# Performance work log

Hardware: AMD Instinct MI355X
Metric: run time of the kernel (lower is better)

Reference implementation:

```python
import jax, jax.numpy as jnp
import numpy as np

B = 64          # number of trees (batch)
N = 131072      # total nodes in batch
H_ENC = 512
H_DEC = 512


def setup_inputs() -> dict:
    key = jax.random.key(0)
    k1, k2, k3, k4, k5 = jax.random.split(key, 5)
    hidden_states = jax.random.normal(k1, (B, H_DEC), dtype=jnp.float32)
    encoder_output = jax.random.normal(k2, (N, H_ENC), dtype=jnp.float32)
    # sorted segment ids encode ragged tree membership (same info as tree_sizes)
    segment_ids = jnp.sort(jax.random.randint(k3, (N,), 0, B)).astype(jnp.int32)
    # linear: nn.Linear(h_dec + h_enc, h_enc, bias=False) -> weight [h_enc, h_dec+h_enc]
    W = jax.random.normal(k4, (H_ENC, H_DEC + H_ENC), dtype=jnp.float32) / np.float32(np.sqrt(H_DEC + H_ENC))
    # v: torch.rand(h_enc, 1)
    v = jax.random.uniform(k5, (H_ENC, 1), dtype=jnp.float32)
    return {"hidden_states": hidden_states, "encoder_output": encoder_output,
            "segment_ids": segment_ids, "W": W, "v": v}


def reference(hidden_states, encoder_output, segment_ids, W, v):
    # repeat each tree's decoder state over its nodes: [N, h_dec]
    repeated = hidden_states[segment_ids]
    # concat score: tanh(Linear([h_dec ; h_enc])) @ v
    cat = jnp.concatenate([repeated, encoder_output], axis=1)      # [N, h_dec+h_enc]
    energy = jnp.tanh(cat @ W.T)                                   # [N, h_enc]
    scores = energy @ v                                            # [N, 1]
    s = scores[:, 0]
    # segment-wise (per-tree) softmax over ragged node groups
    seg_max = jax.ops.segment_max(s, segment_ids, num_segments=B)
    e = jnp.exp(s - seg_max[segment_ids])
    denom = jax.ops.segment_sum(e, segment_ids, num_segments=B)
    att = e / denom[segment_ids]
    return att[:, None]                                            # [N, 1]
```

## Files before the change

### kernel.cpp

```cpp
#include <hip/hip_runtime.h>
#include <math.h>

#define NROWS 131072
#define NSEG  64
#define HH    512

typedef unsigned short u16;
typedef unsigned int   u32;
typedef __attribute__((ext_vector_type(8))) short short8;
typedef __attribute__((ext_vector_type(8))) u16   us8;
typedef __attribute__((ext_vector_type(4))) float f32x4;
typedef __attribute__((ext_vector_type(4))) u32   u32x4;

__device__ __forceinline__ u32 f2u(float f){ union {float f; u32 u;} c; c.f=f; return c.u; }
__device__ __forceinline__ float u2f(u32 u){ union {u32 u; float f;} c; c.u=u; return c.f; }
__device__ __forceinline__ u16 bf16_rne(float f){
  u32 u = f2u(f);
  u32 r = u + 0x7FFFu + ((u >> 16) & 1u);
  return (u16)(r >> 16);
}
__device__ __forceinline__ float fast_tanh(float x){
  float e = __expf(2.0f * x);
  return 1.0f - __fdividef(2.0f, e + 1.0f);
}
__device__ __forceinline__ void gload_lds16(const void* g, void* l) {
  __builtin_amdgcn_global_load_lds((const __attribute__((address_space(1))) void*)g,
                                   (__attribute__((address_space(3))) void*)l, 16, 0, 0);
}

__global__ __launch_bounds__(256)
void hproj_kernel(const float* __restrict__ hidden, const float* __restrict__ W,
                  float* __restrict__ hproj)
{
  const int b    = blockIdx.x >> 2;
  const int q    = blockIdx.x & 3;
  const int tid  = threadIdx.x;
  const int wave = tid >> 6;
  const int lane = tid & 63;
  const float* hrow = hidden + (size_t)b * HH + lane * 8;
  const float4 h0 = *(const float4*)(hrow);
  const float4 h1 = *(const float4*)(hrow + 4);
  for (int j = q * 128 + wave; j < q * 128 + 128; j += 4) {
    const float* wrow = W + (size_t)j * 1024 + lane * 8;
    const float4 w0 = *(const float4*)(wrow);
    const float4 w1 = *(const float4*)(wrow + 4);
    float acc = h0.x*w0.x + h0.y*w0.y + h0.z*w0.z + h0.w*w0.w
              + h1.x*w1.x + h1.y*w1.y + h1.z*w1.z + h1.w*w1.w;
    #pragma unroll
    for (int o = 32; o; o >>= 1) acc += __shfl_xor(acc, o);
    if (lane == 0) hproj[(size_t)b * HH + j] = acc;
  }
}

__global__ __launch_bounds__(256)
void w2split_kernel(const float* __restrict__ W, u16* __restrict__ hi, u16* __restrict__ lo)
{
  const int idx = blockIdx.x * 256 + threadIdx.x;
  const int j = idx >> 9, k = idx & 511;
  const float x = W[(size_t)j * 1024 + 512 + k];
  const u32 u = f2u(x);
  hi[idx] = (u16)(u >> 16);
  lo[idx] = bf16_rne(x - u2f(u & 0xFFFF0000u));
}

__global__ __launch_bounds__(256, 2)
void gemm_fused_kernel(const float* __restrict__ enc,
                       const u16* __restrict__ w2hi, const u16* __restrict__ w2lo,
                       const float* __restrict__ hproj, const float* __restrict__ vvec,
                       const int* __restrict__ seg, float* __restrict__ scores)
{
  __shared__ float sAf[128 * 32];
  __shared__ u16   sBh[256 * 32];
  __shared__ u16   sBl[256 * 32];

  const int tid  = threadIdx.x;
  const int bx   = blockIdx.x;
  const int row0 = (bx >> 1) * 128;
  const int col0 = (bx & 1) * 256;

  const int wave = tid >> 6;
  const int lane = tid & 63;
  const int wrow = (wave >> 1) * 64;
  const int wcol = (wave & 1) * 128;
  const int l15  = lane & 15;
  const int quad = lane >> 4;

  const int arow = tid >> 3;
  const int acol = ((tid & 7) ^ (arow & 6)) * 4;
  const float* gA = enc + (size_t)(row0 + arow) * HH + acol;
  const int awb = (tid >> 6) * 256;

  const int brow = tid >> 2;
  const int bcol = ((tid & 3) ^ ((brow >> 1) & 3)) * 8;
  const u16* gBh = w2hi + (size_t)(col0 + brow) * HH + bcol;
  const u16* gBl = w2lo + (size_t)(col0 + brow) * HH + bcol;
  const int bwb = (tid >> 6) * 512;

  f32x4 acc[4][8];
  #pragma unroll
  for (int i = 0; i < 4; i++)
    #pragma unroll
    for (int j = 0; j < 8; j++)
      acc[i][j] = (f32x4){0.f, 0.f, 0.f, 0.f};

  for (int ks = 0; ks < HH; ks += 32) {
    #pragma unroll
    for (int i = 0; i < 4; i++)
      gload_lds16(gA + (size_t)i * 32 * HH + ks, &sAf[i * 1024 + awb]);
    #pragma unroll
    for (int i = 0; i < 4; i++)
      gload_lds16(gBh + (size_t)i * 64 * HH + ks, &sBh[i * 2048 + bwb]);
    #pragma unroll
    for (int i = 0; i < 4; i++)
      gload_lds16(gBl + (size_t)i * 64 * HH + ks, &sBl[i * 2048 + bwb]);
    __syncthreads();

    short8 ah[4], al[4];
    #pragma unroll
    for (int i = 0; i < 4; i++) {
      const int r  = wrow + i * 16 + l15;
      const int ab = r * 32 + (((2 * quad) ^ (r & 6))) * 4;
      const f32x4 x0 = *(const f32x4*)&sAf[ab];
      const f32x4 x1 = *(const f32x4*)&sAf[ab + 4];
      union { u32x4 w; short8 s; } H, L;
      #pragma unroll
      for (int p = 0; p < 4; p++) {
        const float xa = (p < 2) ? x0[2 * p] : x1[2 * p - 4];
        const float xb = (p < 2) ? x0[2 * p + 1] : x1[2 * p - 3];
        const u32 ua = f2u(xa), ub = f2u(xb);
        H.w[p] = __builtin_amdgcn_perm(ub, ua, 0x07060302u);
        const float ra = xa - u2f(ua & 0xFFFF0000u);
        const float rb = xb - u2f(ub & 0xFFFF0000u);
        L.w[p] = __builtin_amdgcn_perm(f2u(rb), f2u(ra), 0x07060302u);
      }
      ah[i] = H.s;
      al[i] = L.s;
    }

    #pragma unroll
    for (int j = 0; j < 8; j++) {
      const int rr  = wcol + j * 16 + l15;
      const int off = rr * 32 + (quad ^ ((rr >> 1) & 3)) * 8;
      const short8 bh = *(const short8*)&sBh[off];
      const short8 bl = *(const short8*)&sBl[off];
      #pragma unroll
      for (int i = 0; i < 4; i++) {
        acc[i][j] = __builtin_amdgcn_mfma_f32_16x16x32_bf16(ah[i], bh, acc[i][j], 0, 0, 0);
        acc[i][j] = __builtin_amdgcn_mfma_f32_16x16x32_bf16(al[i], bh, acc[i][j], 0, 0, 0);
        acc[i][j] = __builtin_amdgcn_mfma_f32_16x16x32_bf16(ah[i], bl, acc[i][j], 0, 0, 0);
      }
    }
    __syncthreads();
  }

  int   jn[8];
  float vv[8];
  #pragma unroll
  for (int j = 0; j < 8; j++) { jn[j] = col0 + wcol + j * 16 + l15; vv[j] = vvec[jn[j]]; }

  #pragma unroll
  for (int i = 0; i < 4; i++) {
    #pragma unroll
    for (int r = 0; r < 4; r++) {
      const int gn = row0 + wrow + i * 16 + quad * 4 + r;
      const float* hp = hproj + (size_t)seg[gn] * HH;
      float p = 0.f;
      #pragma unroll
      for (int j = 0; j < 8; j++) {
        const float c = acc[i][j][r] + hp[jn[j]];
        p += fast_tanh(c) * vv[j];
      }
      p += __shfl_xor(p, 1);
      p += __shfl_xor(p, 2);
      p += __shfl_xor(p, 4);
      p += __shfl_xor(p, 8);
      if (l15 == 0) atomicAdd(&scores[gn], p);
    }
  }
}

__global__ __launch_bounds__(256)
void seg_softmax_kernel(const float* __restrict__ scores, const int* __restrict__ seg,
                        float* __restrict__ out)
{
  const int b    = blockIdx.x;
  const int tid  = threadIdx.x;
  const int wv   = tid >> 6;
  const int lane = tid & 63;
  __shared__ float red[4];

  int lo = 0, hi = NROWS;
  while (lo < hi) { int mid = (lo + hi) >> 1; if (seg[mid] < b) lo = mid + 1; else hi = mid; }
  const int start = lo;
  lo = 0; hi = NROWS;
  while (lo < hi) { int mid = (lo + hi) >> 1; if (seg[mid] < b + 1) lo = mid + 1; else hi = mid; }
  const int end = lo;

  float lm = -3.4e38f;
  for (int i = start + tid; i < end; i += 256) lm = fmaxf(lm, scores[i]);
  #pragma unroll
  for (int o = 32; o; o >>= 1) lm = fmaxf(lm, __shfl_xor(lm, o));
  if (lane == 0) red[wv] = lm;
  __syncthreads();
  const float gm = fmaxf(fmaxf(red[0], red[1]), fmaxf(red[2], red[3]));
  __syncthreads();

  float ls = 0.f;
  for (int i = start + tid; i < end; i += 256) ls += expf(scores[i] - gm);
  #pragma unroll
  for (int o = 32; o; o >>= 1) ls += __shfl_xor(ls, o);
  if (lane == 0) red[wv] = ls;
  __syncthreads();
  const float denom = red[0] + red[1] + red[2] + red[3];
  const float inv = 1.0f / denom;

  for (int i = start + tid; i < end; i += 256) out[i] = expf(scores[i] - gm) * inv;
}

extern "C" void kernel_launch(void* const* d_in, const int* in_sizes, int n_in,
                              void* d_out, int out_size, void* d_ws, size_t ws_size,
                              hipStream_t stream)
{
  const float* hidden = (const float*)d_in[0];
  const float* enc    = (const float*)d_in[1];
  const int*   seg    = (const int*)d_in[2];
  const float* W      = (const float*)d_in[3];
  const float* vvec   = (const float*)d_in[4];
  float* out = (float*)d_out;

  float* scores = (float*)d_ws;
  float* hproj  = scores + NROWS;
  u16*   w2hi   = (u16*)(hproj + NSEG * HH);
  u16*   w2lo   = w2hi + (size_t)HH * HH;

  hipMemsetAsync(scores, 0, NROWS * sizeof(float), stream);
  hproj_kernel<<<NSEG * 4, 256, 0, stream>>>(hidden, W, hproj);
  w2split_kernel<<<(HH * HH) / 256, 256, 0, stream>>>(W, w2hi, w2lo);
  gemm_fused_kernel<<<(NROWS / 128) * 2, 256, 0, stream>>>(enc, w2hi, w2lo,
                                                           hproj, vvec, seg, scores);
  seg_softmax_kernel<<<NSEG, 256, 0, stream>>>(scores, seg, out);
}
```

Before: 543.1 us.

## Double-buffer pre-converted bf16 A tiles in LDS and load B directly from global

Replaces the global_load_lds staging of fp32 A and the bf16 hi/lo B tiles. A is now prefetched into registers, split once into bf16 hi/lo and written to a double-buffered, padded LDS tile (LDA=40), so one sync per k-step overlaps the next tile's global load with the current MFMAs. Each wave reads its B fragments straight from global memory, which the small, cache-resident W2 allows. The aim is to stop every wave from redoing the A split and to overlap loads with compute, at the cost of more registers for prefetch and B fragments and more global/L2 traffic for B.

Result: slower. 674.1 us (+24.1%).

```diff
diff --git a/kernel.cpp b/kernel.cpp
--- a/kernel.cpp
+++ b/kernel.cpp
@@ -4,6 +4,7 @@
 #define NROWS 131072
 #define NSEG  64
 #define HH    512
+#define LDA   40
 
 typedef unsigned short u16;
 typedef unsigned int   u32;
@@ -22,10 +23,6 @@
 __device__ __forceinline__ float fast_tanh(float x){
   float e = __expf(2.0f * x);
   return 1.0f - __fdividef(2.0f, e + 1.0f);
-}
-__device__ __forceinline__ void gload_lds16(const void* g, void* l) {
-  __builtin_amdgcn_global_load_lds((const __attribute__((address_space(1))) void*)g,
-                                   (__attribute__((address_space(3))) void*)l, 16, 0, 0);
 }
 
 __global__ __launch_bounds__(256)
@@ -63,15 +60,31 @@
   lo[idx] = bf16_rne(x - u2f(u & 0xFFFF0000u));
 }
 
+__device__ __forceinline__ void convert_write(const float* pf, u16* dh, u16* dl)
+{
+  union { u32x4 w; us8 s; } H0, H1, L0, L1;
+  #pragma unroll
+  for (int p = 0; p < 8; p++) {
+    const float xa = pf[2 * p], xb = pf[2 * p + 1];
+    const u32 ua = f2u(xa), ub = f2u(xb);
+    const u32 h = __builtin_amdgcn_perm(ub, ua, 0x07060302u);
+    const float ra = xa - u2f(ua & 0xFFFF0000u);
+    const float rb = xb - u2f(ub & 0xFFFF0000u);
+    const u32 l = __builtin_amdgcn_perm(f2u(rb), f2u(ra), 0x07060302u);
+    if (p < 4) { H0.w[p] = h; L0.w[p] = l; } else { H1.w[p - 4] = h; L1.w[p - 4] = l; }
+  }
+  *(us8*)(dh)     = H0.s;  *(us8*)(dh + 8) = H1.s;
+  *(us8*)(dl)     = L0.s;  *(us8*)(dl + 8) = L1.s;
+}
+
 __global__ __launch_bounds__(256, 2)
 void gemm_fused_kernel(const float* __restrict__ enc,
                        const u16* __restrict__ w2hi, const u16* __restrict__ w2lo,
                        const float* __restrict__ hproj, const float* __restrict__ vvec,
                        const int* __restrict__ seg, float* __restrict__ scores)
 {
-  __shared__ float sAf[128 * 32];
-  __shared__ u16   sBh[256 * 32];
-  __shared__ u16   sBl[256 * 32];
+  __shared__ u16 sAh[2][128 * LDA];
+  __shared__ u16 sAl[2][128 * LDA];
 
   const int tid  = threadIdx.x;
   const int bx   = blockIdx.x;
@@ -85,16 +98,16 @@
   const int l15  = lane & 15;
   const int quad = lane >> 4;
 
-  const int arow = tid >> 3;
-  const int acol = ((tid & 7) ^ (arow & 6)) * 4;
-  const float* gA = enc + (size_t)(row0 + arow) * HH + acol;
-  const int awb = (tid >> 6) * 256;
-
-  const int brow = tid >> 2;
-  const int bcol = ((tid & 3) ^ ((brow >> 1) & 3)) * 8;
-  const u16* gBh = w2hi + (size_t)(col0 + brow) * HH + bcol;
-  const u16* gBl = w2lo + (size_t)(col0 + brow) * HH + bcol;
-  const int bwb = (tid >> 6) * 512;
+  const int sr = tid >> 1;
+  const int sh = (tid & 1) * 16;
+  const float* gA = enc + (size_t)(row0 + sr) * HH + sh;
+  u16* const dh0 = &sAh[0][sr * LDA + sh];
+  u16* const dl0 = &sAl[0][sr * LDA + sh];
+  u16* const dh1 = &sAh[1][sr * LDA + sh];
+  u16* const dl1 = &sAl[1][sr * LDA + sh];
+
+  const u16* gBh = w2hi + (size_t)(col0 + wcol + l15) * HH + quad * 8;
+  const u16* gBl = w2lo + (size_t)(col0 + wcol + l15) * HH + quad * 8;
 
   f32x4 acc[4][8];
   #pragma unroll
@@ -103,51 +116,48 @@
     for (int j = 0; j < 8; j++)
       acc[i][j] = (f32x4){0.f, 0.f, 0.f, 0.f};
 
+  float pf[16];
+  #pragma unroll
+  for (int q = 0; q < 4; q++) *(float4*)&pf[4 * q] = *(const float4*)(gA + 4 * q);
+  convert_write(pf, dh0, dl0);
+  #pragma unroll
+  for (int q = 0; q < 4; q++) *(float4*)&pf[4 * q] = *(const float4*)(gA + 32 + 4 * q);
+  __syncthreads();
+
   for (int ks = 0; ks < HH; ks += 32) {
-    #pragma unroll
-    for (int i = 0; i < 4; i++)
-      gload_lds16(gA + (size_t)i * 32 * HH + ks, &sAf[i * 1024 + awb]);
-    #pragma unroll
-    for (int i = 0; i < 4; i++)
-      gload_lds16(gBh + (size_t)i * 64 * HH + ks, &sBh[i * 2048 + bwb]);
-    #pragma unroll
-    for (int i = 0; i < 4; i++)
-      gload_lds16(gBl + (size_t)i * 64 * HH + ks, &sBl[i * 2048 + bwb]);
-    __syncthreads();
-
-    short8 ah[4], al[4];
-    #pragma unroll
-    for (int i = 0; i < 4; i++) {
-      const int r  = wrow + i * 16 + l15;
-      const int ab = r * 32 + (((2 * quad) ^ (r & 6))) * 4;
-      const f32x4 x0 = *(const f32x4*)&sAf[ab];
-      const f32x4 x1 = *(const f32x4*)&sAf[ab + 4];
-      union { u32x4 w; short8 s; } H, L;
+    const int cur = (ks >> 5) & 1;
+    const u16* cAh = sAh[cur];
+    const u16* cAl = sAl[cur];
+
+    if (ks + 32 < HH) {
+      convert_write(pf, cur ? dh0 : dh1, cur ? dl0 : dl1);
+      if (ks + 64 < HH) {
+        #pragma unroll
+        for (int q = 0; q < 4; q++)
+          *(float4*)&pf[4 * q] = *(const float4*)(gA + ks + 64 + 4 * q);
+      }
+    }
+
+    #pragma unroll
+    for (int jb = 0; jb < 2; jb++) {
+      short8 bh4[4], bl4[4];
       #pragma unroll
-      for (int p = 0; p < 4; p++) {
-        const float xa = (p < 2) ? x0[2 * p] : x1[2 * p - 4];
-        const float xb = (p < 2) ? x0[2 * p + 1] : x1[2 * p - 3];
-        const u32 ua = f2u(xa), ub = f2u(xb);
-        H.w[p] = __builtin_amdgcn_perm(ub, ua, 0x07060302u);
-        const float ra = xa - u2f(ua & 0xFFFF0000u);
-        const float rb = xb - u2f(ub & 0xFFFF0000u);
-        L.w[p] = __builtin_amdgcn_perm(f2u(rb), f2u(ra), 0x07060302u);
-      }
-      ah[i] = H.s;
-      al[i] = L.s;
-    }
-
-    #pragma unroll
-    for (int j = 0; j < 8; j++) {
-      const int rr  = wcol + j * 16 + l15;
-      const int off = rr * 32 + (quad ^ ((rr >> 1) & 3)) * 8;
-      const short8 bh = *(const short8*)&sBh[off];
-      const short8 bl = *(const short8*)&sBl[off];
+      for (int j = 0; j < 4; j++) {
+        const size_t off = (size_t)(jb * 4 + j) * 16 * HH + ks;
+        bh4[j] = *(const short8*)(gBh + off);
+        bl4[j] = *(const short8*)(gBl + off);
+      }
       #pragma unroll
       for (int i = 0; i < 4; i++) {
-        acc[i][j] = __builtin_amdgcn_mfma_f32_16x16x32_bf16(ah[i], bh, acc[i][j], 0, 0, 0);
-        acc[i][j] = __builtin_amdgcn_mfma_f32_16x16x32_bf16(al[i], bh, acc[i][j], 0, 0, 0);
-        acc[i][j] = __builtin_amdgcn_mfma_f32_16x16x32_bf16(ah[i], bl, acc[i][j], 0, 0, 0);
+        const int ar = (wrow + i * 16 + l15) * LDA + quad * 8;
+        const short8 ah = *(const short8*)&cAh[ar];
+        const short8 al = *(const short8*)&cAl[ar];
+        #pragma unroll
+        for (int j = 0; j < 4; j++) {
+          acc[i][jb * 4 + j] = __builtin_amdgcn_mfma_f32_16x16x32_bf16(ah, bh4[j], acc[i][jb * 4 + j], 0, 0, 0);
+          acc[i][jb * 4 + j] = __builtin_amdgcn_mfma_f32_16x16x32_bf16(al, bh4[j], acc[i][jb * 4 + j], 0, 0, 0);
+          acc[i][jb * 4 + j] = __builtin_amdgcn_mfma_f32_16x16x32_bf16(ah, bl4[j], acc[i][jb * 4 + j], 0, 0, 0);
+        }
       }
     }
     __syncthreads();
```

## Double-buffer GEMM LDS tiles, load low-weight bf16 to registers, drop atomics

Applied to the files above, without the earlier changes.

The GEMM main loop now double-buffers the encoder and high-part weight tiles in LDS, issuing the next K-slice's async loads before computing the current one. The low-part weight fragments are read straight from global memory into registers, also prefetched one step ahead, so LDS use drops. Per-wave partial scores go to four separate buffers summed in the softmax kernel, replacing atomics and the memset. The two prep kernels are merged into one launch. In exchange the kernel uses more registers and the softmax reads four times as much score data.

New measurement: 588.5 us. +8.4%, slower.

```diff
diff --git a/kernel.cpp b/kernel.cpp
--- a/kernel.cpp
+++ b/kernel.cpp
@@ -29,12 +29,22 @@
 }
 
 __global__ __launch_bounds__(256)
-void hproj_kernel(const float* __restrict__ hidden, const float* __restrict__ W,
-                  float* __restrict__ hproj)
-{
-  const int b    = blockIdx.x >> 2;
-  const int q    = blockIdx.x & 3;
-  const int tid  = threadIdx.x;
+void prep_kernel(const float* __restrict__ hidden, const float* __restrict__ W,
+                 float* __restrict__ hproj, u16* __restrict__ w2hi, u16* __restrict__ w2lo)
+{
+  const int tid = threadIdx.x;
+  if (blockIdx.x < 1024) {
+    const int idx = blockIdx.x * 256 + tid;
+    const int j = idx >> 9, k = idx & 511;
+    const float x = W[(size_t)j * 1024 + 512 + k];
+    const u32 u = f2u(x);
+    w2hi[idx] = (u16)(u >> 16);
+    w2lo[idx] = bf16_rne(x - u2f(u & 0xFFFF0000u));
+    return;
+  }
+  const int bq   = blockIdx.x - 1024;
+  const int b    = bq >> 2;
+  const int q    = bq & 3;
   const int wave = tid >> 6;
   const int lane = tid & 63;
   const float* hrow = hidden + (size_t)b * HH + lane * 8;
@@ -52,26 +62,14 @@
   }
 }
 
-__global__ __launch_bounds__(256)
-void w2split_kernel(const float* __restrict__ W, u16* __restrict__ hi, u16* __restrict__ lo)
-{
-  const int idx = blockIdx.x * 256 + threadIdx.x;
-  const int j = idx >> 9, k = idx & 511;
-  const float x = W[(size_t)j * 1024 + 512 + k];
-  const u32 u = f2u(x);
-  hi[idx] = (u16)(u >> 16);
-  lo[idx] = bf16_rne(x - u2f(u & 0xFFFF0000u));
-}
-
 __global__ __launch_bounds__(256, 2)
 void gemm_fused_kernel(const float* __restrict__ enc,
                        const u16* __restrict__ w2hi, const u16* __restrict__ w2lo,
                        const float* __restrict__ hproj, const float* __restrict__ vvec,
-                       const int* __restrict__ seg, float* __restrict__ scores)
-{
-  __shared__ float sAf[128 * 32];
-  __shared__ u16   sBh[256 * 32];
-  __shared__ u16   sBl[256 * 32];
+                       const int* __restrict__ seg, float* __restrict__ part)
+{
+  __shared__ float sAf[2][128 * 32];
+  __shared__ u16   sBh[2][256 * 32];
 
   const int tid  = threadIdx.x;
   const int bx   = blockIdx.x;
@@ -93,8 +91,9 @@
   const int brow = tid >> 2;
   const int bcol = ((tid & 3) ^ ((brow >> 1) & 3)) * 8;
   const u16* gBh = w2hi + (size_t)(col0 + brow) * HH + bcol;
-  const u16* gBl = w2lo + (size_t)(col0 + brow) * HH + bcol;
   const int bwb = (tid >> 6) * 512;
+
+  const u16* gBl = w2lo + (size_t)(col0 + wcol + l15) * HH + quad * 8;
 
   f32x4 acc[4][8];
   #pragma unroll
@@ -103,25 +102,41 @@
     for (int j = 0; j < 8; j++)
       acc[i][j] = (f32x4){0.f, 0.f, 0.f, 0.f};
 
+  #pragma unroll
+  for (int i = 0; i < 4; i++)
+    gload_lds16(gA + (size_t)i * 32 * HH, &sAf[0][i * 1024 + awb]);
+  #pragma unroll
+  for (int i = 0; i < 4; i++)
+    gload_lds16(gBh + (size_t)i * 64 * HH, &sBh[0][i * 2048 + bwb]);
+  short8 blC[8], blN[8];
+  #pragma unroll
+  for (int j = 0; j < 8; j++)
+    blC[j] = *(const short8*)(gBl + (size_t)j * 16 * HH);
+  __syncthreads();
+
   for (int ks = 0; ks < HH; ks += 32) {
-    #pragma unroll
-    for (int i = 0; i < 4; i++)
-      gload_lds16(gA + (size_t)i * 32 * HH + ks, &sAf[i * 1024 + awb]);
-    #pragma unroll
-    for (int i = 0; i < 4; i++)
-      gload_lds16(gBh + (size_t)i * 64 * HH + ks, &sBh[i * 2048 + bwb]);
-    #pragma unroll
-    for (int i = 0; i < 4; i++)
-      gload_lds16(gBl + (size_t)i * 64 * HH + ks, &sBl[i * 2048 + bwb]);
-    __syncthreads();
+    const int cur = (ks >> 5) & 1;
+    const int nxt = cur ^ 1;
+
+    if (ks + 32 < HH) {
+      #pragma unroll
+      for (int i = 0; i < 4; i++)
+        gload_lds16(gA + (size_t)i * 32 * HH + ks + 32, &sAf[nxt][i * 1024 + awb]);
+      #pragma unroll
+      for (int i = 0; i < 4; i++)
+        gload_lds16(gBh + (size_t)i * 64 * HH + ks + 32, &sBh[nxt][i * 2048 + bwb]);
+      #pragma unroll
+      for (int j = 0; j < 8; j++)
+        blN[j] = *(const short8*)(gBl + (size_t)j * 16 * HH + ks + 32);
+    }
 
     short8 ah[4], al[4];
     #pragma unroll
     for (int i = 0; i < 4; i++) {
       const int r  = wrow + i * 16 + l15;
       const int ab = r * 32 + (((2 * quad) ^ (r & 6))) * 4;
-      const f32x4 x0 = *(const f32x4*)&sAf[ab];
-      const f32x4 x1 = *(const f32x4*)&sAf[ab + 4];
+      const f32x4 x0 = *(const f32x4*)&sAf[cur][ab];
+      const f32x4 x1 = *(const f32x4*)&sAf[cur][ab + 4];
       union { u32x4 w; short8 s; } H, L;
       #pragma unroll
       for (int p = 0; p < 4; p++) {
@@ -141,8 +156,8 @@
     for (int j = 0; j < 8; j++) {
       const int rr  = wcol + j * 16 + l15;
       const int off = rr * 32 + (quad ^ ((rr >> 1) & 3)) * 8;
-      const short8 bh = *(const short8*)&sBh[off];
-      const short8 bl = *(const short8*)&sBl[off];
+      const short8 bh = *(const short8*)&sBh[cur][off];
+      const short8 bl = blC[j];
       #pragma unroll
       for (int i = 0; i < 4; i++) {
         acc[i][j] = __builtin_amdgcn_mfma_f32_16x16x32_bf16(ah[i], bh, acc[i][j], 0, 0, 0);
@@ -151,6 +166,8 @@
       }
     }
     __syncthreads();
+    #pragma unroll
+    for (int j = 0; j < 8; j++) blC[j] = blN[j];
   }
 
   int   jn[8];
@@ -158,6 +175,7 @@
   #pragma unroll
   for (int j = 0; j < 8; j++) { jn[j] = col0 + wcol + j * 16 + l15; vv[j] = vvec[jn[j]]; }
 
+  float* pout = part + (size_t)((bx & 1) * 2 + (wave & 1)) * NROWS;
   #pragma unroll
   for (int i = 0; i < 4; i++) {
     #pragma unroll
@@ -174,13 +192,13 @@
       p += __shfl_xor(p, 2);
       p += __shfl_xor(p, 4);
       p += __shfl_xor(p, 8);
-      if (l15 == 0) atomicAdd(&scores[gn], p);
+      if (l15 == 0) pout[gn] = p;
     }
   }
 }
 
 __global__ __launch_bounds__(256)
-void seg_softmax_kernel(const float* __restrict__ scores, const int* __restrict__ seg,
+void seg_softmax_kernel(const float* __restrict__ part, const int* __restrict__ seg,
                         float* __restrict__ out)
 {
   const int b    = blockIdx.x;
@@ -197,7 +215,10 @@
   const int end = lo;
 
   float lm = -3.4e38f;
-  for (int i = start + tid; i < end; i += 256) lm = fmaxf(lm, scores[i]);
+  for (int i = start + tid; i < end; i += 256) {
+    const float s = part[i] + part[NROWS + i] + part[2 * NROWS + i] + part[3 * NROWS + i];
+    lm = fmaxf(lm, s);
+  }
   #pragma unroll
   for (int o = 32; o; o >>= 1) lm = fmaxf(lm, __shfl_xor(lm, o));
   if (lane == 0) red[wv] = lm;
@@ -206,7 +227,10 @@
   __syncthreads();
 
   float ls = 0.f;
-  for (int i = start + tid; i < end; i += 256) ls += expf(scores[i] - gm);
+  for (int i = start + tid; i < end; i += 256) {
+    const float s = part[i] + part[NROWS + i] + part[2 * NROWS + i] + part[3 * NROWS + i];
+    ls += expf(s - gm);
+  }
   #pragma unroll
   for (int o = 32; o; o >>= 1) ls += __shfl_xor(ls, o);
   if (lane == 0) red[wv] = ls;
@@ -214,7 +238,10 @@
   const float denom = red[0] + red[1] + red[2] + red[3];
   const float inv = 1.0f / denom;
 
-  for (int i = start + tid; i < end; i += 256) out[i] = expf(scores[i] - gm) * inv;
+  for (int i = start + tid; i < end; i += 256) {
+    const float s = part[i] + part[NROWS + i] + part[2 * NROWS + i] + part[3 * NROWS + i];
+    out[i] = expf(s - gm) * inv;
+  }
 }
 
 extern "C" void kernel_launch(void* const* d_in, const int* in_sizes, int n_in,
@@ -228,15 +255,13 @@
   const float* vvec   = (const float*)d_in[4];
   float* out = (float*)d_out;
 
-  float* scores = (float*)d_ws;
-  float* hproj  = scores + NROWS;
-  u16*   w2hi   = (u16*)(hproj + NSEG * HH);
-  u16*   w2lo   = w2hi + (size_t)HH * HH;
-
-  hipMemsetAsync(scores, 0, NROWS * sizeof(float), stream);
-  hproj_kernel<<<NSEG * 4, 256, 0, stream>>>(hidden, W, hproj);
-  w2split_kernel<<<(HH * HH) / 256, 256, 0, stream>>>(W, w2hi, w2lo);
+  float* part  = (float*)d_ws;
+  float* hproj = part + 4 * (size_t)NROWS;
+  u16*   w2hi  = (u16*)(hproj + NSEG * HH);
+  u16*   w2lo  = w2hi + (size_t)HH * HH;
+
+  prep_kernel<<<1024 + NSEG * 4, 256, 0, stream>>>(hidden, W, hproj, w2hi, w2lo);
   gemm_fused_kernel<<<(NROWS / 128) * 2, 256, 0, stream>>>(enc, w2hi, w2lo,
-                                                           hproj, vvec, seg, scores);
-  seg_softmax_kernel<<<NSEG, 256, 0, stream>>>(scores, seg, out);
-}
+                                                           hproj, vvec, seg, part);
+  seg_softmax_kernel<<<NSEG, 256, 0, stream>>>(part, seg, out);
+}
```
